# Kernel tuning notes

Measured on AMD Instinct MI355X. Metric: run time of the kernel, lower is better.

## Reference

```python
import jax, jax.numpy as jnp
import numpy as np

N, E, D_IN, D_HID, D_OUT = 10000, 160000, 512, 512, 256


def gcn_conv(x, W, src, tgt, n):
    # GCNConv, bias=False: out = D^{-1/2} (A+I) D^{-1/2} (x @ W)
    xw = x @ W                                              # [n, d_out]
    ones = jnp.ones(src.shape[0], dtype=xw.dtype)
    deg = jax.ops.segment_sum(ones, tgt, num_segments=n)    # in-degree incl. self-loop
    dinv = jnp.where(deg > 0, jax.lax.rsqrt(deg), 0.0)
    norm = dinv[src] * dinv[tgt]                            # [e]
    msg = norm[:, None] * xw[src]                           # gather + scale, [e, d_out]
    return jax.ops.segment_sum(msg, tgt, num_segments=n)    # scatter-add to targets


def setup_inputs() -> dict:
    key = jax.random.key(0)
    k1, k2, k3, k4 = jax.random.split(key, 4)
    x = jax.random.normal(k1, (N, D_IN), dtype=jnp.float32)
    edge_index = jax.random.randint(k2, (2, E), 0, N, dtype=jnp.int32)
    W1 = jax.random.normal(k3, (D_IN, D_HID), dtype=jnp.float32) * (1.0 / np.sqrt(D_IN))
    W2 = jax.random.normal(k4, (D_HID, D_OUT), dtype=jnp.float32) * (1.0 / np.sqrt(D_HID))
    return {"x": x, "edge_index": edge_index, "W1": W1, "W2": W2}


def reference(x, edge_index, W1, W2):
    n = x.shape[0]
    loops = jnp.arange(n, dtype=edge_index.dtype)
    src = jnp.concatenate([edge_index[0], loops])  # add self-loops once, reuse both layers
    tgt = jnp.concatenate([edge_index[1], loops])
    h = gcn_conv(x, W1, src, tgt, n)
    h = h ** 2                                     # square activation
    # F.dropout with training=False (eval / inference reference) is identity
    return gcn_conv(h, W2, src, tgt, n)
```

## Files before the change

### kernel.cpp

```cpp
#include <hip/hip_runtime.h>
#include <stdint.h>

typedef __attribute__((ext_vector_type(8))) short bf16x8;
typedef __attribute__((ext_vector_type(4))) short bf16x4;
typedef __attribute__((ext_vector_type(4))) float f32x4;

static __device__ __forceinline__ unsigned short f2bf(float f) {
    unsigned int u = __float_as_uint(f);
    u = u + 0x7FFFu + ((u >> 16) & 1u);
    return (unsigned short)(u >> 16);
}
static __device__ __forceinline__ float bf2f(short b) {
    return __uint_as_float(((unsigned int)(unsigned short)b) << 16);
}

#define GLD_LDS16(g, l) __builtin_amdgcn_global_load_lds( \
    (const __attribute__((address_space(1))) uint32_t*)(g), \
    (__attribute__((address_space(3))) uint32_t*)(l), 16, 0, 0)


__global__ __launch_bounds__(256) void k_setup(
    const int* __restrict__ tgt, int* __restrict__ cnt, int E,
    const float* __restrict__ x, unsigned short* __restrict__ xb, int total4,
    const float* __restrict__ W1, unsigned short* __restrict__ w1t,
    const float* __restrict__ W2, unsigned short* __restrict__ w2t)
{
    const int bid = blockIdx.x;
    const int tid = threadIdx.x;
    if (bid < 625) {
        int e = bid * 256 + tid;
        if (e < E) atomicAdd(&cnt[tgt[e]], 1);
    } else if (bid < 5625) {
        int i = (bid - 625) * 256 + tid;
        if (i < total4) {
            float4 v = ((const float4*)x)[i];
            ushort4 o;
            o.x = f2bf(v.x); o.y = f2bf(v.y); o.z = f2bf(v.z); o.w = f2bf(v.w);
            ((ushort4*)xb)[i] = o;
        }
    } else if (bid < 6649) {
        int idx = (bid - 5625) * 256 + tid;
        int k = idx >> 9, n = idx & 511;
        w1t[(size_t)n * 512 + k] = f2bf(W1[idx]);
    } else {
        int idx = (bid - 6649) * 256 + tid;
        int k = idx >> 8, n = idx & 255;
        w2t[(size_t)n * 512 + k] = f2bf(W2[idx]);
    }
}


__global__ __launch_bounds__(256) void k_scanA(
    const int* __restrict__ cnt, int* __restrict__ row_ptr,
    float* __restrict__ dinv, int* __restrict__ blocksum, int N)
{
    __shared__ int ws[4];
    const int i = blockIdx.x * 256 + threadIdx.x;
    const int lane = threadIdx.x & 63, wid = threadIdx.x >> 6;
    int v = 0;
    if (i < N) { v = cnt[i]; dinv[i] = rsqrtf((float)(v + 1)); }
    int inc = v;
    for (int off = 1; off < 64; off <<= 1) {
        int u = __shfl_up(inc, off, 64);
        if (lane >= off) inc += u;
    }
    if (lane == 63) ws[wid] = inc;
    __syncthreads();
    int wpre = 0;
#pragma unroll
    for (int w = 0; w < 4; ++w) wpre += (w < wid) ? ws[w] : 0;
    if (i < N) row_ptr[i] = wpre + inc - v;
    if (threadIdx.x == 255) blocksum[blockIdx.x] = wpre + inc;
}

__global__ void k_scanB(const int* __restrict__ blocksum, int* __restrict__ blockoff,
                        int* __restrict__ row_ptr, int N, int NB)
{
    const int lane = threadIdx.x;
    int v = (lane < NB) ? blocksum[lane] : 0;
    int inc = v;
    for (int off = 1; off < 64; off <<= 1) {
        int u = __shfl_up(inc, off, 64);
        if (lane >= off) inc += u;
    }
    if (lane < NB) blockoff[lane] = inc - v;
    if (lane == 63) row_ptr[N] = inc;
}

__global__ __launch_bounds__(256) void k_scanC(
    int* __restrict__ row_ptr, int* __restrict__ row_fill,
    const int* __restrict__ blockoff, int N)
{
    const int i = blockIdx.x * 256 + threadIdx.x;
    if (i < N) {
        int rp = row_ptr[i] + blockoff[blockIdx.x];
        row_ptr[i] = rp;
        row_fill[i] = rp;
    }
}

__global__ void k_fill(const int* __restrict__ src, const int* __restrict__ tgt,
                       int* __restrict__ row_fill, int* __restrict__ esrc, int E) {
    int e = blockIdx.x * blockDim.x + threadIdx.x;
    if (e < E) {
        int pos = atomicAdd(&row_fill[tgt[e]], 1);
        esrc[pos] = src[e];
    }
}


template<bool SCALE_ROW>
__global__ __launch_bounds__(256) void k_gemm(
    const short* __restrict__ A,
    const short* __restrict__ Bt,
    const float* __restrict__ dinv,
    unsigned short* __restrict__ C,
    int M, int N, int K, int ncol, int q, int r)
{
    __shared__ char smem[24576];
    char* smA = smem;
    char* smB = smem + 8192;

    const int orig = blockIdx.x;
    const int xcd = orig & 7, loc = orig >> 3;
    const int wg = (xcd < r ? xcd * (q + 1) : r * (q + 1) + (xcd - r) * q) + loc;
    const int rowbase = (wg / ncol) * 64;
    const int colbase = (wg % ncol) * 128;

    const int tid  = threadIdx.x;
    const int lane = tid & 63;
    const int wave = tid >> 6;

    const int lrow = (lane >> 3);
    const int scol = ((lane & 7) ^ lrow) << 3;
    const int rA0 = wave * 8 + lrow;
    int gA0 = rowbase + rA0;          if (gA0 >= M) gA0 = M - 1;
    int gA1 = rowbase + rA0 + 32;     if (gA1 >= M) gA1 = M - 1;
    const size_t offA0 = (size_t)gA0 * K + scol;
    const size_t offA1 = (size_t)gA1 * K + scol;
    size_t offB[4];
#pragma unroll
    for (int c = 0; c < 4; ++c)
        offB[c] = (size_t)(colbase + c * 32 + rA0) * K + scol;

    char* const dA0 = smA + wave * 1024;
    char* const dA1 = smA + 4096 + wave * 1024;
    char* dB[4];
#pragma unroll
    for (int c = 0; c < 4; ++c) dB[c] = smB + c * 4096 + wave * 1024;

    const int wr = (wave >> 1) * 32;
    const int wc = (wave & 1) * 64;
    const int fr = lane & 15;
    const int fs = lane >> 4;

    f32x4 acc[2][4];
#pragma unroll
    for (int m = 0; m < 2; ++m)
#pragma unroll
        for (int n = 0; n < 4; ++n)
            acc[m][n] = (f32x4){0.f, 0.f, 0.f, 0.f};

    for (int k0 = 0; k0 < K; k0 += 64) {
        GLD_LDS16(A + offA0 + k0, dA0);
        GLD_LDS16(A + offA1 + k0, dA1);
#pragma unroll
        for (int c = 0; c < 4; ++c)
            GLD_LDS16(Bt + offB[c] + k0, dB[c]);
        __syncthreads();

        bf16x8 a[2][2], b[4][2];
#pragma unroll
        for (int m = 0; m < 2; ++m)
#pragma unroll
            for (int ks = 0; ks < 2; ++ks) {
                int rr = wr + m * 16 + fr;
                int s = ks * 4 + fs;
                a[m][ks] = *(const bf16x8*)(smA + rr * 128 + ((s ^ (rr & 7)) << 4));
            }
#pragma unroll
        for (int n = 0; n < 4; ++n)
#pragma unroll
            for (int ks = 0; ks < 2; ++ks) {
                int rr = wc + n * 16 + fr;
                int s = ks * 4 + fs;
                b[n][ks] = *(const bf16x8*)(smB + rr * 128 + ((s ^ (rr & 7)) << 4));
            }
#pragma unroll
        for (int m = 0; m < 2; ++m)
#pragma unroll
            for (int n = 0; n < 4; ++n)
#pragma unroll
                for (int ks = 0; ks < 2; ++ks)
                    acc[m][n] = __builtin_amdgcn_mfma_f32_16x16x32_bf16(
                        a[m][ks], b[n][ks], acc[m][n], 0, 0, 0);
        __syncthreads();
    }

    const int orow0 = rowbase + wr + fs * 4;
    const int ocol0 = colbase + wc + fr;
#pragma unroll
    for (int m = 0; m < 2; ++m)
#pragma unroll
        for (int i = 0; i < 4; ++i) {
            int row = orow0 + m * 16 + i;
            if (row < M) {
                float sc = SCALE_ROW ? dinv[row] : 1.0f;
#pragma unroll
                for (int n = 0; n < 4; ++n)
                    C[(size_t)row * N + ocol0 + n * 16] = f2bf(sc * acc[m][n][i]);
            }
        }
}


__global__ __launch_bounds__(256) void k_agg1(
    const unsigned short* __restrict__ xwb,
    const int* __restrict__ row_ptr, const int* __restrict__ esrc,
    const float* __restrict__ dinv,
    unsigned short* __restrict__ hb, int Nn)
{
    const int t = blockIdx.x * 4 + (threadIdx.x >> 6);
    if (t >= Nn) return;
    const int lane = threadIdx.x & 63;
    const float dt = dinv[t];

    float acc[8];
    bf16x8 v = *(const bf16x8*)(xwb + (size_t)t * 512 + lane * 8);
#pragma unroll
    for (int j = 0; j < 8; ++j) acc[j] = bf2f(v[j]);

    int e = row_ptr[t];
    const int e1 = row_ptr[t + 1];
    for (; e + 7 < e1; e += 8) {
        int s[8];
#pragma unroll
        for (int j = 0; j < 8; ++j) s[j] = esrc[e + j];
        bf16x8 u[8];
#pragma unroll
        for (int j = 0; j < 8; ++j)
            u[j] = *(const bf16x8*)(xwb + (size_t)s[j] * 512 + lane * 8);
#pragma unroll
        for (int j = 0; j < 8; ++j)
#pragma unroll
            for (int c = 0; c < 8; ++c) acc[c] += bf2f(u[j][c]);
    }
    for (; e + 3 < e1; e += 4) {
        int s[4];
#pragma unroll
        for (int j = 0; j < 4; ++j) s[j] = esrc[e + j];
        bf16x8 u[4];
#pragma unroll
        for (int j = 0; j < 4; ++j)
            u[j] = *(const bf16x8*)(xwb + (size_t)s[j] * 512 + lane * 8);
#pragma unroll
        for (int j = 0; j < 4; ++j)
#pragma unroll
            for (int c = 0; c < 8; ++c) acc[c] += bf2f(u[j][c]);
    }
    for (; e < e1; ++e) {
        int s = esrc[e];
        bf16x8 u = *(const bf16x8*)(xwb + (size_t)s * 512 + lane * 8);
#pragma unroll
        for (int c = 0; c < 8; ++c) acc[c] += bf2f(u[c]);
    }

    bf16x8 o;
#pragma unroll
    for (int c = 0; c < 8; ++c) {
        float pre = dt * acc[c];
        o[c] = (short)f2bf(dt * pre * pre);
    }
    *(bf16x8*)(hb + (size_t)t * 512 + lane * 8) = o;
}

__global__ __launch_bounds__(256) void k_agg2(
    const unsigned short* __restrict__ xwb,
    const int* __restrict__ row_ptr, const int* __restrict__ esrc,
    const float* __restrict__ dinv,
    float* __restrict__ out, int Nn)
{
    const int t = blockIdx.x * 4 + (threadIdx.x >> 6);
    if (t >= Nn) return;
    const int lane = threadIdx.x & 63;
    const float dt = dinv[t];

    float acc[4];
    bf16x4 v = *(const bf16x4*)(xwb + (size_t)t * 256 + lane * 4);
#pragma unroll
    for (int j = 0; j < 4; ++j) acc[j] = bf2f(v[j]);

    int e = row_ptr[t];
    const int e1 = row_ptr[t + 1];
    for (; e + 7 < e1; e += 8) {
        int s[8];
#pragma unroll
        for (int j = 0; j < 8; ++j) s[j] = esrc[e + j];
        bf16x4 u[8];
#pragma unroll
        for (int j = 0; j < 8; ++j)
            u[j] = *(const bf16x4*)(xwb + (size_t)s[j] * 256 + lane * 4);
#pragma unroll
        for (int j = 0; j < 8; ++j)
#pragma unroll
            for (int c = 0; c < 4; ++c) acc[c] += bf2f(u[j][c]);
    }
    for (; e + 3 < e1; e += 4) {
        int s[4];
#pragma unroll
        for (int j = 0; j < 4; ++j) s[j] = esrc[e + j];
        bf16x4 u[4];
#pragma unroll
        for (int j = 0; j < 4; ++j)
            u[j] = *(const bf16x4*)(xwb + (size_t)s[j] * 256 + lane * 4);
#pragma unroll
        for (int j = 0; j < 4; ++j)
#pragma unroll
            for (int c = 0; c < 4; ++c) acc[c] += bf2f(u[j][c]);
    }
    for (; e < e1; ++e) {
        int s = esrc[e];
        bf16x4 u = *(const bf16x4*)(xwb + (size_t)s * 256 + lane * 4);
#pragma unroll
        for (int c = 0; c < 4; ++c) acc[c] += bf2f(u[c]);
    }

    float4 rout;
    rout.x = dt * acc[0]; rout.y = dt * acc[1];
    rout.z = dt * acc[2]; rout.w = dt * acc[3];
    ((float4*)(out + (size_t)t * 256))[lane] = rout;
}


extern "C" void kernel_launch(void* const* d_in, const int* in_sizes, int n_in,
                              void* d_out, int out_size, void* d_ws, size_t ws_size,
                              hipStream_t stream) {
    const float* x   = (const float*)d_in[0];
    const int*  eidx = (const int*)d_in[1];
    const float* W1  = (const float*)d_in[2];
    const float* W2  = (const float*)d_in[3];
    float* out = (float*)d_out;

    const int DIN = 512, DHID = 512, DOUT = 256;
    const int Nn = in_sizes[0] / DIN;
    const int E  = in_sizes[1] / 2;
    const int* src = eidx;
    const int* tgt = eidx + E;

    char* ws = (char*)d_ws;
    size_t off = 0;
    auto alloc = [&](size_t bytes) -> char* {
        off = (off + 255) & ~(size_t)255;
        char* p = ws + off;
        off += bytes;
        return p;
    };

    int*   cnt      = (int*)  alloc((size_t)Nn * 4);
    int*   row_ptr  = (int*)  alloc((size_t)(Nn + 1) * 4);
    int*   row_fill = (int*)  alloc((size_t)Nn * 4);
    float* dinv     = (float*)alloc((size_t)Nn * 4);
    int*   esrc     = (int*)  alloc((size_t)E * 4);
    int*   blocksum = (int*)  alloc(64 * 4);
    int*   blockoff = (int*)  alloc(64 * 4);
    unsigned short* xb   = (unsigned short*)alloc((size_t)Nn * DIN * 2);
    unsigned short* w1t  = (unsigned short*)alloc((size_t)DIN * DHID * 2);
    unsigned short* w2t  = (unsigned short*)alloc((size_t)DHID * DOUT * 2);
    unsigned short* xwb  = (unsigned short*)alloc((size_t)Nn * DHID * 2);
    unsigned short* hb   = (unsigned short*)alloc((size_t)Nn * DHID * 2);
    unsigned short* xw2b = (unsigned short*)alloc((size_t)Nn * DOUT * 2);

    hipMemsetAsync(cnt, 0, (size_t)Nn * 4, stream);

    const int total4 = Nn * DIN / 4;
    const int NB = (Nn + 255) / 256;
    k_setup<<<7161, 256, 0, stream>>>(tgt, cnt, E, x, xb, total4, W1, w1t, W2, w2t);
    k_scanA<<<NB, 256, 0, stream>>>(cnt, row_ptr, dinv, blocksum, Nn);
    k_scanB<<<1, 64, 0, stream>>>(blocksum, blockoff, row_ptr, Nn, NB);
    k_scanC<<<NB, 256, 0, stream>>>(row_ptr, row_fill, blockoff, Nn);
    k_fill<<<(E + 255) / 256, 256, 0, stream>>>(src, tgt, row_fill, esrc, E);

    {
        const int nrow = (Nn + 63) / 64, ncol = DHID / 128;
        const int nwg = nrow * ncol;
        k_gemm<true><<<nwg, 256, 0, stream>>>(
            (const short*)xb, (const short*)w1t, dinv, xwb,
            Nn, DHID, DIN, ncol, nwg >> 3, nwg & 7);
    }
    k_agg1<<<(Nn + 3) / 4, 256, 0, stream>>>(xwb, row_ptr, esrc, dinv, hb, Nn);

    {
        const int nrow = (Nn + 63) / 64, ncol = DOUT / 128;
        const int nwg = nrow * ncol;
        k_gemm<false><<<nwg, 256, 0, stream>>>(
            (const short*)hb, (const short*)w2t, dinv, xw2b,
            Nn, DOUT, DHID, ncol, nwg >> 3, nwg & 7);
    }
    k_agg2<<<(Nn + 3) / 4, 256, 0, stream>>>(xw2b, row_ptr, esrc, dinv, out, Nn);
}
```

Baseline: 99.45 us.

## Fuse CSR setup, scans and fill into one persistent kernel with grid barriers

Replaces the five preprocessing launches (setup, three scan stages, fill) with a single persistent kernel of 512 blocks that loops over the old work items and separates the phases with a software grid barrier built on atomics. The cross-block offset for the scan is computed by each block directly from the blocksum array, which removes the single-wave scanB kernel. The aim is to cut launch overhead and inter-kernel gaps. In exchange, the barrier relies on all 512 blocks being co-resident, and the spin-waits plus the reduced grid size for the conversion work may cost throughput.

```diff
diff --git a/kernel.cpp b/kernel.cpp
--- a/kernel.cpp
+++ b/kernel.cpp
@@ -4,6 +4,8 @@
 typedef __attribute__((ext_vector_type(8))) short bf16x8;
 typedef __attribute__((ext_vector_type(4))) short bf16x4;
 typedef __attribute__((ext_vector_type(4))) float f32x4;
+
+#define NBCO 512
 
 static __device__ __forceinline__ unsigned short f2bf(float f) {
     unsigned int u = __float_as_uint(f);
@@ -19,90 +21,105 @@
     (__attribute__((address_space(3))) uint32_t*)(l), 16, 0, 0)
 
 
-__global__ __launch_bounds__(256) void k_setup(
-    const int* __restrict__ tgt, int* __restrict__ cnt, int E,
+static __device__ __forceinline__ void gbar(int* bar, int& epoch_l) {
+    __syncthreads();
+    if (threadIdx.x == 0) {
+        ++epoch_l;
+        int prev = __hip_atomic_fetch_add(&bar[0], 1, __ATOMIC_ACQ_REL,
+                                          __HIP_MEMORY_SCOPE_AGENT);
+        if (prev == NBCO - 1) {
+            __hip_atomic_store(&bar[0], 0, __ATOMIC_RELAXED,
+                               __HIP_MEMORY_SCOPE_AGENT);
+            __hip_atomic_store(&bar[1], epoch_l, __ATOMIC_RELEASE,
+                               __HIP_MEMORY_SCOPE_AGENT);
+        } else {
+            while (__hip_atomic_load(&bar[1], __ATOMIC_ACQUIRE,
+                                     __HIP_MEMORY_SCOPE_AGENT) < epoch_l)
+                __builtin_amdgcn_s_sleep(2);
+        }
+    }
+    __syncthreads();
+}
+
+
+__global__ __launch_bounds__(256, 2) void k_csr(
+    const int* __restrict__ src, const int* __restrict__ tgt, int E,
     const float* __restrict__ x, unsigned short* __restrict__ xb, int total4,
     const float* __restrict__ W1, unsigned short* __restrict__ w1t,
-    const float* __restrict__ W2, unsigned short* __restrict__ w2t)
+    const float* __restrict__ W2, unsigned short* __restrict__ w2t,
+    int* bar, int* __restrict__ cnt,
+    int* __restrict__ row_ptr, int* __restrict__ row_fill,
+    float* __restrict__ dinv, int* __restrict__ blocksum,
+    int* __restrict__ esrc, int N)
 {
     const int bid = blockIdx.x;
     const int tid = threadIdx.x;
-    if (bid < 625) {
-        int e = bid * 256 + tid;
-        if (e < E) atomicAdd(&cnt[tgt[e]], 1);
-    } else if (bid < 5625) {
-        int i = (bid - 625) * 256 + tid;
-        if (i < total4) {
-            float4 v = ((const float4*)x)[i];
-            ushort4 o;
-            o.x = f2bf(v.x); o.y = f2bf(v.y); o.z = f2bf(v.z); o.w = f2bf(v.w);
-            ((ushort4*)xb)[i] = o;
-        }
-    } else if (bid < 6649) {
-        int idx = (bid - 5625) * 256 + tid;
-        int k = idx >> 9, n = idx & 511;
-        w1t[(size_t)n * 512 + k] = f2bf(W1[idx]);
-    } else {
-        int idx = (bid - 6649) * 256 + tid;
-        int k = idx >> 8, n = idx & 255;
-        w2t[(size_t)n * 512 + k] = f2bf(W2[idx]);
-    }
-}
-
-
-__global__ __launch_bounds__(256) void k_scanA(
-    const int* __restrict__ cnt, int* __restrict__ row_ptr,
-    float* __restrict__ dinv, int* __restrict__ blocksum, int N)
-{
-    __shared__ int ws[4];
-    const int i = blockIdx.x * 256 + threadIdx.x;
-    const int lane = threadIdx.x & 63, wid = threadIdx.x >> 6;
-    int v = 0;
-    if (i < N) { v = cnt[i]; dinv[i] = rsqrtf((float)(v + 1)); }
-    int inc = v;
-    for (int off = 1; off < 64; off <<= 1) {
-        int u = __shfl_up(inc, off, 64);
-        if (lane >= off) inc += u;
-    }
-    if (lane == 63) ws[wid] = inc;
-    __syncthreads();
-    int wpre = 0;
-#pragma unroll
-    for (int w = 0; w < 4; ++w) wpre += (w < wid) ? ws[w] : 0;
-    if (i < N) row_ptr[i] = wpre + inc - v;
-    if (threadIdx.x == 255) blocksum[blockIdx.x] = wpre + inc;
-}
-
-__global__ void k_scanB(const int* __restrict__ blocksum, int* __restrict__ blockoff,
-                        int* __restrict__ row_ptr, int N, int NB)
-{
-    const int lane = threadIdx.x;
-    int v = (lane < NB) ? blocksum[lane] : 0;
-    int inc = v;
-    for (int off = 1; off < 64; off <<= 1) {
-        int u = __shfl_up(inc, off, 64);
-        if (lane >= off) inc += u;
-    }
-    if (lane < NB) blockoff[lane] = inc - v;
-    if (lane == 63) row_ptr[N] = inc;
-}
-
-__global__ __launch_bounds__(256) void k_scanC(
-    int* __restrict__ row_ptr, int* __restrict__ row_fill,
-    const int* __restrict__ blockoff, int N)
-{
-    const int i = blockIdx.x * 256 + threadIdx.x;
-    if (i < N) {
-        int rp = row_ptr[i] + blockoff[blockIdx.x];
-        row_ptr[i] = rp;
-        row_fill[i] = rp;
-    }
-}
-
-__global__ void k_fill(const int* __restrict__ src, const int* __restrict__ tgt,
-                       int* __restrict__ row_fill, int* __restrict__ esrc, int E) {
-    int e = blockIdx.x * blockDim.x + threadIdx.x;
-    if (e < E) {
+    int epoch_l = 0;
+
+    for (int vb = bid; vb < 7161; vb += NBCO) {
+        if (vb < 625) {
+            int e = vb * 256 + tid;
+            if (e < E) atomicAdd(&cnt[tgt[e]], 1);
+        } else if (vb < 5625) {
+            int i = (vb - 625) * 256 + tid;
+            if (i < total4) {
+                float4 v = ((const float4*)x)[i];
+                ushort4 o;
+                o.x = f2bf(v.x); o.y = f2bf(v.y); o.z = f2bf(v.z); o.w = f2bf(v.w);
+                ((ushort4*)xb)[i] = o;
+            }
+        } else if (vb < 6649) {
+            int idx = (vb - 5625) * 256 + tid;
+            int k = idx >> 9, n = idx & 511;
+            w1t[(size_t)n * 512 + k] = f2bf(W1[idx]);
+        } else {
+            int idx = (vb - 6649) * 256 + tid;
+            int k = idx >> 8, n = idx & 255;
+            w2t[(size_t)n * 512 + k] = f2bf(W2[idx]);
+        }
+    }
+    gbar(bar, epoch_l);
+
+    const int nbs = (N + 255) >> 8;
+    __shared__ int ws4[4];
+    if (bid < nbs) {
+        const int i = bid * 256 + tid;
+        const int lane = tid & 63, wid2 = tid >> 6;
+        int v = 0;
+        if (i < N) { v = cnt[i]; dinv[i] = rsqrtf((float)(v + 1)); }
+        int inc = v;
+        for (int off2 = 1; off2 < 64; off2 <<= 1) {
+            int u = __shfl_up(inc, off2, 64);
+            if (lane >= off2) inc += u;
+        }
+        if (lane == 63) ws4[wid2] = inc;
+        __syncthreads();
+        int wpre = 0;
+#pragma unroll
+        for (int w = 0; w < 4; ++w) wpre += (w < wid2) ? ws4[w] : 0;
+        if (i < N) row_ptr[i] = wpre + inc - v;
+        if (tid == 255) blocksum[bid] = wpre + inc;
+    }
+    gbar(bar, epoch_l);
+
+    if (bid < nbs) {
+        int off = 0;
+        for (int w = 0; w < bid; ++w) off += blocksum[w];
+        const int i = bid * 256 + tid;
+        if (i < N) {
+            int rp = row_ptr[i] + off;
+            row_ptr[i] = rp;
+            row_fill[i] = rp;
+        }
+        if (bid == 0 && tid == 0) {
+            int tot = 0;
+            for (int w = 0; w < nbs; ++w) tot += blocksum[w];
+            row_ptr[N] = tot;
+        }
+    }
+    gbar(bar, epoch_l);
+
+    for (int e = bid * 256 + tid; e < E; e += NBCO * 256) {
         int pos = atomicAdd(&row_fill[tgt[e]], 1);
         esrc[pos] = src[e];
     }
@@ -356,13 +373,13 @@
         return p;
     };
 
+    int*   bar      = (int*)  alloc(8);
     int*   cnt      = (int*)  alloc((size_t)Nn * 4);
     int*   row_ptr  = (int*)  alloc((size_t)(Nn + 1) * 4);
     int*   row_fill = (int*)  alloc((size_t)Nn * 4);
     float* dinv     = (float*)alloc((size_t)Nn * 4);
     int*   esrc     = (int*)  alloc((size_t)E * 4);
     int*   blocksum = (int*)  alloc(64 * 4);
-    int*   blockoff = (int*)  alloc(64 * 4);
     unsigned short* xb   = (unsigned short*)alloc((size_t)Nn * DIN * 2);
     unsigned short* w1t  = (unsigned short*)alloc((size_t)DIN * DHID * 2);
     unsigned short* w2t  = (unsigned short*)alloc((size_t)DHID * DOUT * 2);
@@ -370,15 +387,13 @@
     unsigned short* hb   = (unsigned short*)alloc((size_t)Nn * DHID * 2);
     unsigned short* xw2b = (unsigned short*)alloc((size_t)Nn * DOUT * 2);
 
-    hipMemsetAsync(cnt, 0, (size_t)Nn * 4, stream);
+    hipMemsetAsync(bar, 0, (size_t)256 + (size_t)Nn * 4, stream);
 
     const int total4 = Nn * DIN / 4;
-    const int NB = (Nn + 255) / 256;
-    k_setup<<<7161, 256, 0, stream>>>(tgt, cnt, E, x, xb, total4, W1, w1t, W2, w2t);
-    k_scanA<<<NB, 256, 0, stream>>>(cnt, row_ptr, dinv, blocksum, Nn);
-    k_scanB<<<1, 64, 0, stream>>>(blocksum, blockoff, row_ptr, Nn, NB);
-    k_scanC<<<NB, 256, 0, stream>>>(row_ptr, row_fill, blockoff, Nn);
-    k_fill<<<(E + 255) / 256, 256, 0, stream>>>(src, tgt, row_fill, esrc, E);
+    k_csr<<<NBCO, 256, 0, stream>>>(src, tgt, E, x, xb, total4,
+                                    W1, w1t, W2, w2t,
+                                    bar, cnt, row_ptr, row_fill, dinv,
+                                    blocksum, esrc, Nn);
 
     {
         const int nrow = (Nn + 63) / 64, ncol = DHID / 128;
```

New measurement: 258.6 us. 2.6x slower.

## Store GEMM outputs in 128-column blocked layout and split aggregation by column block

Applied to the files above, without the earlier changes.

The GEMM epilogue now writes its output as column-blocked panels of 128 columns, each [N,128]. The aggregation kernels launch one grid slice per column block, and each lane gathers a single 32-bit word (two bf16) instead of 16- or 8-byte vectors. The intent is that each block's working set of 2.5 MB fits better in cache during the random neighbour gathers. The cost is more blocks and reloading esrc/row_ptr once per column block. The separate single-block scan kernel is removed, and each scanC block now sums the preceding block totals itself; agg2 also uses nontemporal stores for the output.

```diff
diff --git a/kernel.cpp b/kernel.cpp
--- a/kernel.cpp
+++ b/kernel.cpp
@@ -2,8 +2,8 @@
 #include <stdint.h>
 
 typedef __attribute__((ext_vector_type(8))) short bf16x8;
-typedef __attribute__((ext_vector_type(4))) short bf16x4;
 typedef __attribute__((ext_vector_type(4))) float f32x4;
+typedef __attribute__((ext_vector_type(2))) float f32x2;
 
 static __device__ __forceinline__ unsigned short f2bf(float f) {
     unsigned int u = __float_as_uint(f);
@@ -12,6 +12,12 @@
 }
 static __device__ __forceinline__ float bf2f(short b) {
     return __uint_as_float(((unsigned int)(unsigned short)b) << 16);
+}
+static __device__ __forceinline__ float bflo(unsigned int v) {
+    return __uint_as_float(v << 16);
+}
+static __device__ __forceinline__ float bfhi(unsigned int v) {
+    return __uint_as_float(v & 0xffff0000u);
 }
 
 #define GLD_LDS16(g, l) __builtin_amdgcn_global_load_lds( \
@@ -73,29 +79,23 @@
     if (threadIdx.x == 255) blocksum[blockIdx.x] = wpre + inc;
 }
 
-__global__ void k_scanB(const int* __restrict__ blocksum, int* __restrict__ blockoff,
-                        int* __restrict__ row_ptr, int N, int NB)
-{
-    const int lane = threadIdx.x;
-    int v = (lane < NB) ? blocksum[lane] : 0;
-    int inc = v;
-    for (int off = 1; off < 64; off <<= 1) {
-        int u = __shfl_up(inc, off, 64);
-        if (lane >= off) inc += u;
-    }
-    if (lane < NB) blockoff[lane] = inc - v;
-    if (lane == 63) row_ptr[N] = inc;
-}
-
 __global__ __launch_bounds__(256) void k_scanC(
     int* __restrict__ row_ptr, int* __restrict__ row_fill,
-    const int* __restrict__ blockoff, int N)
-{
-    const int i = blockIdx.x * 256 + threadIdx.x;
+    const int* __restrict__ blocksum, int N, int nbs)
+{
+    const int bid = blockIdx.x;
+    int off = 0;
+    for (int w = 0; w < bid; ++w) off += blocksum[w];
+    const int i = bid * 256 + threadIdx.x;
     if (i < N) {
-        int rp = row_ptr[i] + blockoff[blockIdx.x];
+        int rp = row_ptr[i] + off;
         row_ptr[i] = rp;
         row_fill[i] = rp;
+    }
+    if (bid == 0 && threadIdx.x == 0) {
+        int tot = 0;
+        for (int w = 0; w < nbs; ++w) tot += blocksum[w];
+        row_ptr[N] = tot;
     }
 }
 
@@ -197,8 +197,9 @@
         __syncthreads();
     }
 
+    unsigned short* Cq = C + (size_t)(colbase >> 7) * M * 128;
     const int orow0 = rowbase + wr + fs * 4;
-    const int ocol0 = colbase + wc + fr;
+    const int ocol0 = wc + fr;
 #pragma unroll
     for (int m = 0; m < 2; ++m)
 #pragma unroll
@@ -208,27 +209,31 @@
                 float sc = SCALE_ROW ? dinv[row] : 1.0f;
 #pragma unroll
                 for (int n = 0; n < 4; ++n)
-                    C[(size_t)row * N + ocol0 + n * 16] = f2bf(sc * acc[m][n][i]);
+                    Cq[(size_t)row * 128 + ocol0 + n * 16] = f2bf(sc * acc[m][n][i]);
             }
         }
 }
 
 
 __global__ __launch_bounds__(256) void k_agg1(
-    const unsigned short* __restrict__ xwb,
+    const unsigned int* __restrict__ xwb,
     const int* __restrict__ row_ptr, const int* __restrict__ esrc,
     const float* __restrict__ dinv,
-    unsigned short* __restrict__ hb, int Nn)
-{
-    const int t = blockIdx.x * 4 + (threadIdx.x >> 6);
+    unsigned int* __restrict__ hb,
+    int Nn, int nbpb)
+{
+    const int blk = blockIdx.x / nbpb;
+    const int t = (blockIdx.x - blk * nbpb) * 4 + (threadIdx.x >> 6);
     if (t >= Nn) return;
     const int lane = threadIdx.x & 63;
     const float dt = dinv[t];
-
-    float acc[8];
-    bf16x8 v = *(const bf16x8*)(xwb + (size_t)t * 512 + lane * 8);
-#pragma unroll
-    for (int j = 0; j < 8; ++j) acc[j] = bf2f(v[j]);
+    const unsigned int* xq = xwb + (size_t)blk * Nn * 64 + lane;
+
+    float a0, a1;
+    {
+        unsigned int v = xq[(size_t)t * 64];
+        a0 = bflo(v); a1 = bfhi(v);
+    }
 
     int e = row_ptr[t];
     const int e1 = row_ptr[t + 1];
@@ -236,59 +241,54 @@
         int s[8];
 #pragma unroll
         for (int j = 0; j < 8; ++j) s[j] = esrc[e + j];
-        bf16x8 u[8];
-#pragma unroll
-        for (int j = 0; j < 8; ++j)
-            u[j] = *(const bf16x8*)(xwb + (size_t)s[j] * 512 + lane * 8);
-#pragma unroll
-        for (int j = 0; j < 8; ++j)
-#pragma unroll
-            for (int c = 0; c < 8; ++c) acc[c] += bf2f(u[j][c]);
+        unsigned int u[8];
+#pragma unroll
+        for (int j = 0; j < 8; ++j) u[j] = xq[(size_t)s[j] * 64];
+#pragma unroll
+        for (int j = 0; j < 8; ++j) { a0 += bflo(u[j]); a1 += bfhi(u[j]); }
     }
     for (; e + 3 < e1; e += 4) {
         int s[4];
 #pragma unroll
         for (int j = 0; j < 4; ++j) s[j] = esrc[e + j];
-        bf16x8 u[4];
-#pragma unroll
-        for (int j = 0; j < 4; ++j)
-            u[j] = *(const bf16x8*)(xwb + (size_t)s[j] * 512 + lane * 8);
-#pragma unroll
-        for (int j = 0; j < 4; ++j)
-#pragma unroll
-            for (int c = 0; c < 8; ++c) acc[c] += bf2f(u[j][c]);
+        unsigned int u[4];
+#pragma unroll
+        for (int j = 0; j < 4; ++j) u[j] = xq[(size_t)s[j] * 64];
+#pragma unroll
+        for (int j = 0; j < 4; ++j) { a0 += bflo(u[j]); a1 += bfhi(u[j]); }
     }
     for (; e < e1; ++e) {
-        int s = esrc[e];
-        bf16x8 u = *(const bf16x8*)(xwb + (size_t)s * 512 + lane * 8);
-#pragma unroll
-        for (int c = 0; c < 8; ++c) acc[c] += bf2f(u[c]);
-    }
-
-    bf16x8 o;
-#pragma unroll
-    for (int c = 0; c < 8; ++c) {
-        float pre = dt * acc[c];
-        o[c] = (short)f2bf(dt * pre * pre);
-    }
-    *(bf16x8*)(hb + (size_t)t * 512 + lane * 8) = o;
-}
+        unsigned int u = xq[(size_t)esrc[e] * 64];
+        a0 += bflo(u); a1 += bfhi(u);
+    }
+
+    float p0 = dt * a0, p1 = dt * a1;
+    p0 = dt * p0 * p0;
+    p1 = dt * p1 * p1;
+    hb[(size_t)t * 256 + blk * 64 + lane] =
+        ((unsigned int)f2bf(p1) << 16) | (unsigned int)f2bf(p0);
+}
+
 
 __global__ __launch_bounds__(256) void k_agg2(
-    const unsigned short* __restrict__ xwb,
+    const unsigned int* __restrict__ xwb,
     const int* __restrict__ row_ptr, const int* __restrict__ esrc,
     const float* __restrict__ dinv,
-    float* __restrict__ out, int Nn)
-{
-    const int t = blockIdx.x * 4 + (threadIdx.x >> 6);
+    float* __restrict__ out,
+    int Nn, int nbpb)
+{
+    const int blk = blockIdx.x / nbpb;
+    const int t = (blockIdx.x - blk * nbpb) * 4 + (threadIdx.x >> 6);
     if (t >= Nn) return;
     const int lane = threadIdx.x & 63;
     const float dt = dinv[t];
-
-    float acc[4];
-    bf16x4 v = *(const bf16x4*)(xwb + (size_t)t * 256 + lane * 4);
-#pragma unroll
-    for (int j = 0; j < 4; ++j) acc[j] = bf2f(v[j]);
+    const unsigned int* xq = xwb + (size_t)blk * Nn * 64 + lane;
+
+    float a0, a1;
+    {
+        unsigned int v = xq[(size_t)t * 64];
+        a0 = bflo(v); a1 = bfhi(v);
+    }
 
     int e = row_ptr[t];
     const int e1 = row_ptr[t + 1];
@@ -296,39 +296,30 @@
         int s[8];
 #pragma unroll
         for (int j = 0; j < 8; ++j) s[j] = esrc[e + j];
-        bf16x4 u[8];
-#pragma unroll
-        for (int j = 0; j < 8; ++j)
-            u[j] = *(const bf16x4*)(xwb + (size_t)s[j] * 256 + lane * 4);
-#pragma unroll
-        for (int j = 0; j < 8; ++j)
-#pragma unroll
-            for (int c = 0; c < 4; ++c) acc[c] += bf2f(u[j][c]);
+        unsigned int u[8];
+#pragma unroll
+        for (int j = 0; j < 8; ++j) u[j] = xq[(size_t)s[j] * 64];
+#pragma unroll
+        for (int j = 0; j < 8; ++j) { a0 += bflo(u[j]); a1 += bfhi(u[j]); }
     }
     for (; e + 3 < e1; e += 4) {
         int s[4];
 #pragma unroll
         for (int j = 0; j < 4; ++j) s[j] = esrc[e + j];
-        bf16x4 u[4];
-#pragma unroll
-        for (int j = 0; j < 4; ++j)
-            u[j] = *(const bf16x4*)(xwb + (size_t)s[j] * 256 + lane * 4);
-#pragma unroll
-        for (int j = 0; j < 4; ++j)
-#pragma unroll
-            for (int c = 0; c < 4; ++c) acc[c] += bf2f(u[j][c]);
+        unsigned int u[4];
+#pragma unroll
+        for (int j = 0; j < 4; ++j) u[j] = xq[(size_t)s[j] * 64];
+#pragma unroll
+        for (int j = 0; j < 4; ++j) { a0 += bflo(u[j]); a1 += bfhi(u[j]); }
     }
     for (; e < e1; ++e) {
-        int s = esrc[e];
-        bf16x4 u = *(const bf16x4*)(xwb + (size_t)s * 256 + lane * 4);
-#pragma unroll
-        for (int c = 0; c < 4; ++c) acc[c] += bf2f(u[c]);
-    }
-
-    float4 rout;
-    rout.x = dt * acc[0]; rout.y = dt * acc[1];
-    rout.z = dt * acc[2]; rout.w = dt * acc[3];
-    ((float4*)(out + (size_t)t * 256))[lane] = rout;
+        unsigned int u = xq[(size_t)esrc[e] * 64];
+        a0 += bflo(u); a1 += bfhi(u);
+    }
+
+    f32x2 r;
+    r[0] = dt * a0; r[1] = dt * a1;
+    __builtin_nontemporal_store(r, (f32x2*)(out + (size_t)t * 256 + blk * 128 + lane * 2));
 }
 
 
@@ -362,7 +353,6 @@
     float* dinv     = (float*)alloc((size_t)Nn * 4);
     int*   esrc     = (int*)  alloc((size_t)E * 4);
     int*   blocksum = (int*)  alloc(64 * 4);
-    int*   blockoff = (int*)  alloc(64 * 4);
     unsigned short* xb   = (unsigned short*)alloc((size_t)Nn * DIN * 2);
     unsigned short* w1t  = (unsigned short*)alloc((size_t)DIN * DHID * 2);
     unsigned short* w2t  = (unsigned short*)alloc((size_t)DHID * DOUT * 2);
@@ -370,15 +360,16 @@
     unsigned short* hb   = (unsigned short*)alloc((size_t)Nn * DHID * 2);
     unsigned short* xw2b = (unsigned short*)alloc((size_t)Nn * DOUT * 2);
 
-    hipMemsetAsync(cnt, 0, (size_t)Nn * 4, stream);
+    (void)hipMemsetAsync(cnt, 0, (size_t)Nn * 4, stream);
 
     const int total4 = Nn * DIN / 4;
     const int NB = (Nn + 255) / 256;
     k_setup<<<7161, 256, 0, stream>>>(tgt, cnt, E, x, xb, total4, W1, w1t, W2, w2t);
     k_scanA<<<NB, 256, 0, stream>>>(cnt, row_ptr, dinv, blocksum, Nn);
-    k_scanB<<<1, 64, 0, stream>>>(blocksum, blockoff, row_ptr, Nn, NB);
-    k_scanC<<<NB, 256, 0, stream>>>(row_ptr, row_fill, blockoff, Nn);
+    k_scanC<<<NB, 256, 0, stream>>>(row_ptr, row_fill, blocksum, Nn, NB);
     k_fill<<<(E + 255) / 256, 256, 0, stream>>>(src, tgt, row_fill, esrc, E);
+
+    const int nbpb = (Nn + 3) / 4;
 
     {
         const int nrow = (Nn + 63) / 64, ncol = DHID / 128;
@@ -387,7 +378,8 @@
             (const short*)xb, (const short*)w1t, dinv, xwb,
             Nn, DHID, DIN, ncol, nwg >> 3, nwg & 7);
     }
-    k_agg1<<<(Nn + 3) / 4, 256, 0, stream>>>(xwb, row_ptr, esrc, dinv, hb, Nn);
+    k_agg1<<<4 * nbpb, 256, 0, stream>>>((const unsigned int*)xwb, row_ptr, esrc,
+                                         dinv, (unsigned int*)hb, Nn, nbpb);
 
     {
         const int nrow = (Nn + 63) / 64, ncol = DOUT / 128;
@@ -396,5 +388,6 @@
             (const short*)hb, (const short*)w2t, dinv, xw2b,
             Nn, DOUT, DHID, ncol, nwg >> 3, nwg & 7);
     }
-    k_agg2<<<(Nn + 3) / 4, 256, 0, stream>>>(xw2b, row_ptr, esrc, dinv, out, Nn);
-}
+    k_agg2<<<2 * nbpb, 256, 0, stream>>>((const unsigned int*)xw2b, row_ptr, esrc,
+                                         dinv, out, Nn, nbpb);
+}
```

Measured after the change: 101.3 us. About the same (+1.9%).
